# Optimization experiments

Hardware: AMD Instinct MI355X
Metric: run time of the kernel (lower is better)

The kernel has to match this reference:

```python
import jax, jax.numpy as jnp
import numpy as np

N, E = 50000, 800000          # nodes, edges
IN_CH, HID, HEADS = 256, 32, 4  # conv1: 256 -> 32x4; conv2: 128 -> 128 (1 head)
NEG_SLOPE = 0.2               # PyG GATConv default LeakyReLU slope


def setup_inputs() -> dict:
    key = jax.random.key(0)
    ks = jax.random.split(key, 9)
    H1 = HID * HEADS
    p = lambda k, shape, s: jax.random.normal(k, shape, jnp.float32) * s
    return {
        "x": jax.random.normal(ks[0], (N, IN_CH), jnp.float32),
        "src": jax.random.randint(ks[1], (E,), 0, N, dtype=jnp.int32),
        "dst": jax.random.randint(ks[2], (E,), 0, N, dtype=jnp.int32),
        "W1": p(ks[3], (IN_CH, H1), (2.0 / IN_CH) ** 0.5),
        "att_src1": p(ks[4], (HEADS, HID), 0.1),
        "att_dst1": p(ks[5], (HEADS, HID), 0.1),
        "b1": jnp.zeros((H1,), jnp.float32),
        "W2": p(ks[6], (H1, H1), (2.0 / H1) ** 0.5),
        "att_src2": p(ks[7], (1, H1), 0.1),
        "att_dst2": p(ks[8], (1, H1), 0.1),
        "b2": jnp.zeros((H1,), jnp.float32),
    }


def _gat_conv(x, src, dst, W, a_src, a_dst, b):
    """PyG-style GATConv: project, per-edge attention, segment softmax over dst, scatter-sum."""
    n = x.shape[0]
    H, C = a_src.shape
    xp = (x @ W).reshape(n, H, C)                      # [N,H,C]
    al_s = jnp.sum(xp * a_src, axis=-1)                # [N,H]
    al_d = jnp.sum(xp * a_dst, axis=-1)                # [N,H]
    e = jax.nn.leaky_relu(al_s[src] + al_d[dst], NEG_SLOPE)   # [E,H]
    m = jax.lax.stop_gradient(jax.ops.segment_max(e, dst, num_segments=n))
    ex = jnp.exp(e - m[dst])                           # stable segment softmax
    z = jax.ops.segment_sum(ex, dst, num_segments=n)
    alpha = ex / (z[dst] + 1e-16)                      # [E,H]
    out = jax.ops.segment_sum(xp[src] * alpha[..., None], dst, num_segments=n)
    return out.reshape(n, H * C) + b


def reference(x, src, dst, W1, att_src1, att_dst1, b1, W2, att_src2, att_dst2, b2):
    n = x.shape[0]
    loops = jnp.arange(n, dtype=src.dtype)             # add_self_loops=True (PyG default)
    s = jnp.concatenate([src, loops])
    d = jnp.concatenate([dst, loops])
    # eval mode: dropout is identity
    h = jax.nn.elu(_gat_conv(x, s, d, W1, att_src1, att_dst1, b1))
    return _gat_conv(h, s, d, W2, att_src2, att_dst2, b2)
```

## Files before the change

kernel.cpp:

```cpp
#include <hip/hip_runtime.h>

#define NN 50000
#define NE 800000
#define NEG 0.2f

constexpr int NB1 = (NN + 255) / 256;

__device__ __forceinline__ float lrelu(float x) { return x > 0.f ? x : NEG * x; }

__global__ void hist_k(const int* __restrict__ dst, int* __restrict__ deg) {
    int i = blockIdx.x * 256 + threadIdx.x;
    if (i < NE) atomicAdd(&deg[dst[i]], 1);
}

__global__ void scan1_k(const int* __restrict__ deg, int* __restrict__ roff,
                        int* __restrict__ bsum) {
    __shared__ int s[256];
    int t = threadIdx.x;
    int i = blockIdx.x * 256 + t;
    int v = (i < NN) ? deg[i] : 0;
    s[t] = v; __syncthreads();
    for (int off = 1; off < 256; off <<= 1) {
        int add = (t >= off) ? s[t - off] : 0;
        __syncthreads();
        s[t] += add;
        __syncthreads();
    }
    if (i < NN) roff[i] = s[t] - v;
    if (t == 255) bsum[blockIdx.x] = s[255];
}

__global__ void scan2_k(const int* __restrict__ bsum, int* __restrict__ boff,
                        int* __restrict__ roff) {
    __shared__ int s[256];
    int t = threadIdx.x;
    int v = (t < NB1) ? bsum[t] : 0;
    s[t] = v; __syncthreads();
    for (int off = 1; off < 256; off <<= 1) {
        int add = (t >= off) ? s[t - off] : 0;
        __syncthreads();
        s[t] += add;
        __syncthreads();
    }
    if (t < NB1) boff[t] = s[t] - v;
    if (t == 255) roff[NN] = s[255];
}

__global__ void scan3_k(int* __restrict__ roff, const int* __restrict__ boff,
                        int* __restrict__ cursor) {
    int i = blockIdx.x * 256 + threadIdx.x;
    if (i < NN) {
        int v = roff[i] + boff[blockIdx.x];
        roff[i] = v;
        cursor[i] = v;
    }
}

template <bool WITH_DST>
__global__ void fill_k(const int* __restrict__ src, const int* __restrict__ dst,
                       int* __restrict__ cursor, int* __restrict__ csr,
                       int* __restrict__ dstOf) {
    int i = blockIdx.x * 256 + threadIdx.x;
    if (i < NE) {
        int d = dst[i];
        int p = atomicAdd(&cursor[d], 1);
        csr[p] = src[i];
        if (WITH_DST) dstOf[p] = d;
    }
}

__global__ void wt1_k(const int* __restrict__ csr, const int* __restrict__ dstOf,
                      const float* __restrict__ als, const float* __restrict__ ald,
                      float* __restrict__ w) {
    int p = blockIdx.x * 256 + threadIdx.x;
    if (p >= NE) return;
    int s = csr[p], d = dstOf[p];
    float4 av = *reinterpret_cast<const float4*>(&als[s * 4]);
    float4 dv = *reinterpret_cast<const float4*>(&ald[d * 4]);
    float4 wv;
    wv.x = __expf(lrelu(av.x + dv.x));
    wv.y = __expf(lrelu(av.y + dv.y));
    wv.z = __expf(lrelu(av.z + dv.z));
    wv.w = __expf(lrelu(av.w + dv.w));
    *reinterpret_cast<float4*>(&w[(size_t)p * 4]) = wv;
}

__global__ void wt2_k(const int* __restrict__ csr, const int* __restrict__ dstOf,
                      const float* __restrict__ als, const float* __restrict__ ald,
                      float* __restrict__ w) {
    int p = blockIdx.x * 256 + threadIdx.x;
    if (p >= NE) return;
    w[p] = __expf(lrelu(als[csr[p]] + ald[dstOf[p]]));
}

template <int K, int HEADS>
__global__ __launch_bounds__(256) void gemm_k(const float* __restrict__ A,
                                              const float* __restrict__ W,
                                              const float* __restrict__ att_s,
                                              const float* __restrict__ att_d,
                                              float* __restrict__ O,
                                              float* __restrict__ als,
                                              float* __restrict__ ald, int M) {
    __shared__ float sAT[32][68];
    __shared__ float sB[32][128];
    int row0 = blockIdx.x * 64;
    int t = threadIdx.x;
    int rg = t >> 5;
    int cg = t & 31;
    float acc[8][4] = {};
    for (int k0 = 0; k0 < K; k0 += 32) {
        #pragma unroll
        for (int p = 0; p < 2; ++p) {
            int r = p * 32 + (t >> 3);
            int kk4 = (t & 7) * 4;
            int gr = row0 + r;
            float4 v = make_float4(0.f, 0.f, 0.f, 0.f);
            if (gr < M) v = *reinterpret_cast<const float4*>(&A[(size_t)gr * K + k0 + kk4]);
            sAT[kk4 + 0][r] = v.x;
            sAT[kk4 + 1][r] = v.y;
            sAT[kk4 + 2][r] = v.z;
            sAT[kk4 + 3][r] = v.w;
        }
        #pragma unroll
        for (int p = 0; p < 4; ++p) {
            int kr = p * 8 + (t >> 5);
            int c4 = (t & 31) * 4;
            *reinterpret_cast<float4*>(&sB[kr][c4]) =
                *reinterpret_cast<const float4*>(&W[(size_t)(k0 + kr) * 128 + c4]);
        }
        __syncthreads();
        #pragma unroll
        for (int kk = 0; kk < 32; ++kk) {
            float4 a0 = *reinterpret_cast<const float4*>(&sAT[kk][rg * 8]);
            float4 a1 = *reinterpret_cast<const float4*>(&sAT[kk][rg * 8 + 4]);
            float4 bv = *reinterpret_cast<const float4*>(&sB[kk][cg * 4]);
            float ar[8] = {a0.x, a0.y, a0.z, a0.w, a1.x, a1.y, a1.z, a1.w};
            #pragma unroll
            for (int r = 0; r < 8; ++r) {
                acc[r][0] += ar[r] * bv.x;
                acc[r][1] += ar[r] * bv.y;
                acc[r][2] += ar[r] * bv.z;
                acc[r][3] += ar[r] * bv.w;
            }
        }
        __syncthreads();
    }
    constexpr int GROUP = 32 / HEADS;
    float4 as4 = *reinterpret_cast<const float4*>(&att_s[cg * 4]);
    float4 ad4 = *reinterpret_cast<const float4*>(&att_d[cg * 4]);
    #pragma unroll
    for (int r = 0; r < 8; ++r) {
        int gr = row0 + rg * 8 + r;
        float4 o = make_float4(acc[r][0], acc[r][1], acc[r][2], acc[r][3]);
        float ps = o.x * as4.x + o.y * as4.y + o.z * as4.z + o.w * as4.w;
        float pd = o.x * ad4.x + o.y * ad4.y + o.z * ad4.z + o.w * ad4.w;
        #pragma unroll
        for (int m = 1; m < GROUP; m <<= 1) {
            ps += __shfl_xor(ps, m, 64);
            pd += __shfl_xor(pd, m, 64);
        }
        if (gr < M) {
            *reinterpret_cast<float4*>(&O[(size_t)gr * 128 + cg * 4]) = o;
            if ((cg & (GROUP - 1)) == 0) {
                int h = cg / GROUP;
                als[(size_t)gr * HEADS + h] = ps;
                ald[(size_t)gr * HEADS + h] = pd;
            }
        }
    }
}

template <int HEADS>
__global__ __launch_bounds__(256) void aggf_k(const int* __restrict__ roff,
                                              const int* __restrict__ csr,
                                              const float* __restrict__ w,
                                              const float* __restrict__ xp,
                                              const float* __restrict__ als,
                                              const float* __restrict__ ald,
                                              const float* __restrict__ b,
                                              float* __restrict__ outp, int doElu) {
    int node = (blockIdx.x * 256 + threadIdx.x) >> 6;
    int lane = threadIdx.x & 63;
    if (node >= NN) return;
    int hw = lane >> 5;
    int l  = lane & 31;
    int h  = (HEADS == 4) ? (l >> 3) : 0;
    int e0 = roff[node], e1 = roff[node + 1];

    float selfw;
    if (HEADS == 4) {
        float4 adv = *reinterpret_cast<const float4*>(&ald[node * 4]);
        float4 sv  = *reinterpret_cast<const float4*>(&als[node * 4]);
        float adh = (h == 0) ? adv.x : (h == 1) ? adv.y : (h == 2) ? adv.z : adv.w;
        float svh = (h == 0) ? sv.x  : (h == 1) ? sv.y  : (h == 2) ? sv.z  : sv.w;
        selfw = __expf(lrelu(svh + adh));
    } else {
        selfw = __expf(lrelu(als[node] + ald[node]));
    }

    float aA0 = 0.f, aA1 = 0.f, aA2 = 0.f, aA3 = 0.f, zA = 0.f;
    float aB0 = 0.f, aB1 = 0.f, aB2 = 0.f, aB3 = 0.f, zB = 0.f;
    if (hw == 0) {
        zA = selfw;
        float4 v = *reinterpret_cast<const float4*>(&xp[(size_t)node * 128 + 4 * l]);
        aA0 = selfw * v.x; aA1 = selfw * v.y; aA2 = selfw * v.z; aA3 = selfw * v.w;
    }
    for (int j = e0 + hw; j < e1; j += 8) {
        int i1 = j + 2, i2 = j + 4, i3 = j + 6;
        bool p1 = i1 < e1, p2 = i2 < e1, p3 = i3 < e1;
        int j1 = p1 ? i1 : j, j2 = p2 ? i2 : j, j3 = p3 ? i3 : j;
        int s0 = csr[j], s1 = csr[j1], s2 = csr[j2], s3 = csr[j3];
        float w0, w1v, w2v, w3v;
        if (HEADS == 4) {
            w0  = w[(size_t)j  * 4 + h];
            w1v = w[(size_t)j1 * 4 + h];
            w2v = w[(size_t)j2 * 4 + h];
            w3v = w[(size_t)j3 * 4 + h];
        } else {
            w0 = w[j]; w1v = w[j1]; w2v = w[j2]; w3v = w[j3];
        }
        w1v = p1 ? w1v : 0.f;
        w2v = p2 ? w2v : 0.f;
        w3v = p3 ? w3v : 0.f;
        float4 v0 = *reinterpret_cast<const float4*>(&xp[(size_t)s0 * 128 + 4 * l]);
        float4 v1 = *reinterpret_cast<const float4*>(&xp[(size_t)s1 * 128 + 4 * l]);
        float4 v2 = *reinterpret_cast<const float4*>(&xp[(size_t)s2 * 128 + 4 * l]);
        float4 v3 = *reinterpret_cast<const float4*>(&xp[(size_t)s3 * 128 + 4 * l]);
        zA += w0;  aA0 += w0 * v0.x;  aA1 += w0 * v0.y;  aA2 += w0 * v0.z;  aA3 += w0 * v0.w;
        zA += w1v; aA0 += w1v * v1.x; aA1 += w1v * v1.y; aA2 += w1v * v1.z; aA3 += w1v * v1.w;
        zB += w2v; aB0 += w2v * v2.x; aB1 += w2v * v2.y; aB2 += w2v * v2.z; aB3 += w2v * v2.w;
        zB += w3v; aB0 += w3v * v3.x; aB1 += w3v * v3.y; aB2 += w3v * v3.z; aB3 += w3v * v3.w;
    }
    float a0 = aA0 + aB0, a1 = aA1 + aB1, a2 = aA2 + aB2, a3 = aA3 + aB3, z = zA + zB;
    a0 += __shfl_xor(a0, 32, 64);
    a1 += __shfl_xor(a1, 32, 64);
    a2 += __shfl_xor(a2, 32, 64);
    a3 += __shfl_xor(a3, 32, 64);
    z  += __shfl_xor(z, 32, 64);
    if (hw == 0) {
        float inv = 1.f / (z + 1e-16f);
        float4 bb = *reinterpret_cast<const float4*>(&b[4 * l]);
        float o0 = a0 * inv + bb.x, o1 = a1 * inv + bb.y;
        float o2 = a2 * inv + bb.z, o3 = a3 * inv + bb.w;
        if (doElu) {
            o0 = o0 > 0.f ? o0 : expm1f(o0);
            o1 = o1 > 0.f ? o1 : expm1f(o1);
            o2 = o2 > 0.f ? o2 : expm1f(o2);
            o3 = o3 > 0.f ? o3 : expm1f(o3);
        }
        *reinterpret_cast<float4*>(&outp[(size_t)node * 128 + 4 * l]) =
            make_float4(o0, o1, o2, o3);
    }
}

__global__ __launch_bounds__(256) void agg1_k(const int* __restrict__ roff,
                                              const int* __restrict__ csr,
                                              const float* __restrict__ xp,
                                              const float* __restrict__ als,
                                              const float* __restrict__ ald,
                                              const float* __restrict__ b,
                                              float* __restrict__ hout) {
    int node = (blockIdx.x * 256 + threadIdx.x) >> 6;
    int lane = threadIdx.x & 63;
    if (node >= NN) return;
    int hw = lane >> 5;
    int l  = lane & 31;
    int h  = l >> 3;
    int e0 = roff[node], e1 = roff[node + 1];

    float4 adv = *reinterpret_cast<const float4*>(&ald[node * 4]);
    float4 sv  = *reinterpret_cast<const float4*>(&als[node * 4]);
    float adh = (h == 0) ? adv.x : (h == 1) ? adv.y : (h == 2) ? adv.z : adv.w;
    float svh = (h == 0) ? sv.x  : (h == 1) ? sv.y  : (h == 2) ? sv.z  : sv.w;

    float aA0 = 0.f, aA1 = 0.f, aA2 = 0.f, aA3 = 0.f, zA = 0.f;
    float aB0 = 0.f, aB1 = 0.f, aB2 = 0.f, aB3 = 0.f, zB = 0.f;
    if (hw == 0) {
        float ex = __expf(lrelu(svh + adh));
        zA = ex;
        float4 v = *reinterpret_cast<const float4*>(&xp[(size_t)node * 128 + 4 * l]);
        aA0 = ex * v.x; aA1 = ex * v.y; aA2 = ex * v.z; aA3 = ex * v.w;
    }
    for (int j = e0 + hw; j < e1; j += 4) {
        int sA = csr[j];
        int jB = j + 2;
        bool hasB = jB < e1;
        int sB = hasB ? csr[jB] : sA;
        float4 avA = *reinterpret_cast<const float4*>(&als[sA * 4]);
        float4 avB = *reinterpret_cast<const float4*>(&als[sB * 4]);
        float alA = (h == 0) ? avA.x : (h == 1) ? avA.y : (h == 2) ? avA.z : avA.w;
        float alB = (h == 0) ? avB.x : (h == 1) ? avB.y : (h == 2) ? avB.z : avB.w;
        float exA = __expf(lrelu(alA + adh));
        float exB = hasB ? __expf(lrelu(alB + adh)) : 0.f;
        float4 vA = *reinterpret_cast<const float4*>(&xp[(size_t)sA * 128 + 4 * l]);
        float4 vB = *reinterpret_cast<const float4*>(&xp[(size_t)sB * 128 + 4 * l]);
        zA += exA; aA0 += exA * vA.x; aA1 += exA * vA.y; aA2 += exA * vA.z; aA3 += exA * vA.w;
        zB += exB; aB0 += exB * vB.x; aB1 += exB * vB.y; aB2 += exB * vB.z; aB3 += exB * vB.w;
    }
    float a0 = aA0 + aB0, a1 = aA1 + aB1, a2 = aA2 + aB2, a3 = aA3 + aB3, z = zA + zB;
    a0 += __shfl_xor(a0, 32, 64);
    a1 += __shfl_xor(a1, 32, 64);
    a2 += __shfl_xor(a2, 32, 64);
    a3 += __shfl_xor(a3, 32, 64);
    z  += __shfl_xor(z, 32, 64);
    if (hw == 0) {
        float inv = 1.f / (z + 1e-16f);
        float4 bb = *reinterpret_cast<const float4*>(&b[4 * l]);
        float o0 = a0 * inv + bb.x, o1 = a1 * inv + bb.y;
        float o2 = a2 * inv + bb.z, o3 = a3 * inv + bb.w;
        o0 = o0 > 0.f ? o0 : expm1f(o0);
        o1 = o1 > 0.f ? o1 : expm1f(o1);
        o2 = o2 > 0.f ? o2 : expm1f(o2);
        o3 = o3 > 0.f ? o3 : expm1f(o3);
        *reinterpret_cast<float4*>(&hout[(size_t)node * 128 + 4 * l]) =
            make_float4(o0, o1, o2, o3);
    }
}

__global__ __launch_bounds__(256) void agg2_k(const int* __restrict__ roff,
                                              const int* __restrict__ csr,
                                              const float* __restrict__ xp,
                                              const float* __restrict__ als,
                                              const float* __restrict__ ald,
                                              const float* __restrict__ b,
                                              float* __restrict__ out) {
    int node = (blockIdx.x * 256 + threadIdx.x) >> 6;
    int lane = threadIdx.x & 63;
    if (node >= NN) return;
    int hw = lane >> 5;
    int l  = lane & 31;
    int e0 = roff[node], e1 = roff[node + 1];
    float ad = ald[node];
    float sl = als[node];

    float aA0 = 0.f, aA1 = 0.f, aA2 = 0.f, aA3 = 0.f, zA = 0.f;
    float aB0 = 0.f, aB1 = 0.f, aB2 = 0.f, aB3 = 0.f, zB = 0.f;
    if (hw == 0) {
        float ex = __expf(lrelu(sl + ad));
        zA = ex;
        float4 v = *reinterpret_cast<const float4*>(&xp[(size_t)node * 128 + 4 * l]);
        aA0 = ex * v.x; aA1 = ex * v.y; aA2 = ex * v.z; aA3 = ex * v.w;
    }
    for (int j = e0 + hw; j < e1; j += 4) {
        int sA = csr[j];
        int jB = j + 2;
        bool hasB = jB < e1;
        int sB = hasB ? csr[jB] : sA;
        float alA = als[sA];
        float alB = als[sB];
        float exA = __expf(lrelu(alA + ad));
        float exB = hasB ? __expf(lrelu(alB + ad)) : 0.f;
        float4 vA = *reinterpret_cast<const float4*>(&xp[(size_t)sA * 128 + 4 * l]);
        float4 vB = *reinterpret_cast<const float4*>(&xp[(size_t)sB * 128 + 4 * l]);
        zA += exA; aA0 += exA * vA.x; aA1 += exA * vA.y; aA2 += exA * vA.z; aA3 += exA * vA.w;
        zB += exB; aB0 += exB * vB.x; aB1 += exB * vB.y; aB2 += exB * vB.z; aB3 += exB * vB.w;
    }
    float a0 = aA0 + aB0, a1 = aA1 + aB1, a2 = aA2 + aB2, a3 = aA3 + aB3, z = zA + zB;
    a0 += __shfl_xor(a0, 32, 64);
    a1 += __shfl_xor(a1, 32, 64);
    a2 += __shfl_xor(a2, 32, 64);
    a3 += __shfl_xor(a3, 32, 64);
    z  += __shfl_xor(z, 32, 64);
    if (hw == 0) {
        float inv = 1.f / (z + 1e-16f);
        float4 bb = *reinterpret_cast<const float4*>(&b[4 * l]);
        *reinterpret_cast<float4*>(&out[(size_t)node * 128 + 4 * l]) =
            make_float4(a0 * inv + bb.x, a1 * inv + bb.y, a2 * inv + bb.z, a3 * inv + bb.w);
    }
}

extern "C" void kernel_launch(void* const* d_in, const int* in_sizes, int n_in,
                              void* d_out, int out_size, void* d_ws, size_t ws_size,
                              hipStream_t stream) {
    const float* x   = (const float*)d_in[0];
    const int*   src = (const int*)d_in[1];
    const int*   dst = (const int*)d_in[2];
    const float* W1  = (const float*)d_in[3];
    const float* as1 = (const float*)d_in[4];
    const float* ad1 = (const float*)d_in[5];
    const float* b1  = (const float*)d_in[6];
    const float* W2  = (const float*)d_in[7];
    const float* as2 = (const float*)d_in[8];
    const float* ad2 = (const float*)d_in[9];
    const float* b2  = (const float*)d_in[10];
    float* out = (float*)d_out;

    char* ws = (char*)d_ws;
    size_t off = 0;
    auto alloc = [&](size_t bytes) {
        size_t o = off;
        off = (off + bytes + 255) & ~(size_t)255;
        return o;
    };
    int*   roff   = (int*)(ws + alloc((NN + 1) * 4));
    int*   cursor = (int*)(ws + alloc(NN * 4));
    int*   deg    = (int*)(ws + alloc(NN * 4));
    int*   bsum   = (int*)(ws + alloc(256 * 4));
    int*   boff   = (int*)(ws + alloc(256 * 4));
    int*   csr    = (int*)(ws + alloc((size_t)NE * 4));
    float* xp1    = (float*)(ws + alloc((size_t)NN * 128 * 4));
    float* als1   = (float*)(ws + alloc((size_t)NN * 4 * 4));
    float* ald1   = (float*)(ws + alloc((size_t)NN * 4 * 4));
    float* hbuf   = (float*)(ws + alloc((size_t)NN * 128 * 4));
    int*   dstOf  = (int*)(ws + alloc((size_t)NE * 4));
    float* w1     = (float*)(ws + alloc((size_t)NE * 4 * 4));
    float* w2     = w1;
    bool fast = (off <= ws_size);

    float* xp2  = xp1;
    float* als2 = als1;
    float* ald2 = ald1;

    hipMemsetAsync(deg, 0, (size_t)NN * 4, stream);
    hist_k<<<(NE + 255) / 256, 256, 0, stream>>>(dst, deg);
    scan1_k<<<NB1, 256, 0, stream>>>(deg, roff, bsum);
    scan2_k<<<1, 256, 0, stream>>>(bsum, boff, roff);
    scan3_k<<<NB1, 256, 0, stream>>>(roff, boff, cursor);
    int eGrid = (NE + 255) / 256;
    if (fast) fill_k<true><<<eGrid, 256, 0, stream>>>(src, dst, cursor, csr, dstOf);
    else      fill_k<false><<<eGrid, 256, 0, stream>>>(src, dst, cursor, csr, dstOf);

    int aggGrid  = (NN + 3) / 4;
    int gemmGrid = (NN + 63) / 64;

    gemm_k<256, 4><<<gemmGrid, 256, 0, stream>>>(x, W1, as1, ad1, xp1, als1, ald1, NN);
    if (fast) {
        wt1_k<<<eGrid, 256, 0, stream>>>(csr, dstOf, als1, ald1, w1);
        aggf_k<4><<<aggGrid, 256, 0, stream>>>(roff, csr, w1, xp1, als1, ald1, b1, hbuf, 1);
    } else {
        agg1_k<<<aggGrid, 256, 0, stream>>>(roff, csr, xp1, als1, ald1, b1, hbuf);
    }

    gemm_k<128, 1><<<gemmGrid, 256, 0, stream>>>(hbuf, W2, as2, ad2, xp2, als2, ald2, NN);
    if (fast) {
        wt2_k<<<eGrid, 256, 0, stream>>>(csr, dstOf, als2, ald2, w2);
        aggf_k<1><<<aggGrid, 256, 0, stream>>>(roff, csr, w2, xp2, als2, ald2, b2, out, 0);
    } else {
        agg2_k<<<aggGrid, 256, 0, stream>>>(roff, csr, xp2, als2, ald2, b2, out);
    }
}
```

Baseline: 408.1 us.

## Replace FP32 projection GEMMs with split-bf16 MFMA GEMMs

Adds a kernel that pre-splits each weight matrix into high and low bf16 parts, transposed. The projection GEMMs then run on MFMA 16x16x32 bf16 instructions using three products (hi*hi, lo*hi, hi*lo), which recovers near-FP32 accuracy, and the attention dot-products are fused into the epilogue. The aim is to replace the scalar FP32 GEMM path with matrix-core throughput. In exchange it adds per-call bf16 splitting of the activations and weights, extra LDS traffic, and two small weight-split launches, with slightly lower precision than true FP32.

```diff
diff --git a/kernel.cpp b/kernel.cpp
--- a/kernel.cpp
+++ b/kernel.cpp
@@ -7,6 +7,14 @@
 constexpr int NB1 = (NN + 255) / 256;
 
 __device__ __forceinline__ float lrelu(float x) { return x > 0.f ? x : NEG * x; }
+
+typedef __attribute__((ext_vector_type(8))) short short8v;
+typedef __attribute__((ext_vector_type(4))) float f32x4;
+
+__device__ __forceinline__ ushort f2bf(float x) {
+    unsigned u = __float_as_uint(x);
+    return (ushort)((u + 0x7FFFu + ((u >> 16) & 1u)) >> 16);
+}
 
 __global__ void hist_k(const int* __restrict__ dst, int* __restrict__ deg) {
     int i = blockIdx.x * 256 + threadIdx.x;
@@ -67,6 +75,19 @@
         csr[p] = src[i];
         if (WITH_DST) dstOf[p] = d;
     }
+}
+
+__global__ void wsplit_k(const float* __restrict__ W, ushort* __restrict__ WTh,
+                         ushort* __restrict__ WTl, int K) {
+    int idx = blockIdx.x * 256 + threadIdx.x;
+    if (idx >= K * 128) return;
+    int c = idx / K;
+    int k = idx - c * K;
+    float v = W[(size_t)k * 128 + c];
+    ushort h = f2bf(v);
+    float hf = __uint_as_float(((unsigned)h) << 16);
+    WTh[idx] = h;
+    WTl[idx] = f2bf(v - hf);
 }
 
 __global__ void wt1_k(const int* __restrict__ csr, const int* __restrict__ dstOf,
@@ -91,6 +112,131 @@
     int p = blockIdx.x * 256 + threadIdx.x;
     if (p >= NE) return;
     w[p] = __expf(lrelu(als[csr[p]] + ald[dstOf[p]]));
+}
+
+template <int K, int HEADS>
+__global__ __launch_bounds__(256) void gemm_mfma_k(const float* __restrict__ A,
+                                                   const ushort* __restrict__ WTh,
+                                                   const ushort* __restrict__ WTl,
+                                                   const float* __restrict__ att_s,
+                                                   const float* __restrict__ att_d,
+                                                   float* __restrict__ O,
+                                                   float* __restrict__ als,
+                                                   float* __restrict__ ald, int M) {
+    __shared__ ushort sAh[64][40];
+    __shared__ ushort sAl[64][40];
+    __shared__ ushort sWh[128][40];
+    __shared__ ushort sWl[128][40];
+    int t = threadIdx.x;
+    int w = t >> 6;
+    int l = t & 63;
+    int r16 = l & 15, kg = l >> 4;
+    int row0 = blockIdx.x * 64;
+
+    f32x4 acc[8] = {};
+
+    for (int k0 = 0; k0 < K; k0 += 32) {
+        #pragma unroll
+        for (int p = 0; p < 2; ++p) {
+            int idx = p * 256 + t;
+            int r = idx >> 3, kk = (idx & 7) * 4;
+            int gr = row0 + r;
+            float4 v = make_float4(0.f, 0.f, 0.f, 0.f);
+            if (gr < M) v = *reinterpret_cast<const float4*>(&A[(size_t)gr * K + k0 + kk]);
+            ushort h0 = f2bf(v.x), h1 = f2bf(v.y), h2 = f2bf(v.z), h3 = f2bf(v.w);
+            short4 hv = make_short4((short)h0, (short)h1, (short)h2, (short)h3);
+            float f0 = __uint_as_float(((unsigned)h0) << 16);
+            float f1 = __uint_as_float(((unsigned)h1) << 16);
+            float f2 = __uint_as_float(((unsigned)h2) << 16);
+            float f3 = __uint_as_float(((unsigned)h3) << 16);
+            short4 lv = make_short4((short)f2bf(v.x - f0), (short)f2bf(v.y - f1),
+                                    (short)f2bf(v.z - f2), (short)f2bf(v.w - f3));
+            *reinterpret_cast<short4*>(&sAh[r][kk]) = hv;
+            *reinterpret_cast<short4*>(&sAl[r][kk]) = lv;
+        }
+        {
+            int c = t & 127, kh = (t >> 7) * 16;
+            const int4* gh = reinterpret_cast<const int4*>(&WTh[(size_t)c * K + k0 + kh]);
+            const int4* gl = reinterpret_cast<const int4*>(&WTl[(size_t)c * K + k0 + kh]);
+            int4 a0 = gh[0], a1 = gh[1];
+            int4 b0 = gl[0], b1 = gl[1];
+            *reinterpret_cast<int4*>(&sWh[c][kh])     = a0;
+            *reinterpret_cast<int4*>(&sWh[c][kh + 8]) = a1;
+            *reinterpret_cast<int4*>(&sWl[c][kh])     = b0;
+            *reinterpret_cast<int4*>(&sWl[c][kh + 8]) = b1;
+        }
+        __syncthreads();
+        short8v ah = *reinterpret_cast<const short8v*>(&sAh[w * 16 + r16][kg * 8]);
+        short8v al_ = *reinterpret_cast<const short8v*>(&sAl[w * 16 + r16][kg * 8]);
+        #pragma unroll
+        for (int ct = 0; ct < 8; ++ct) {
+            short8v bh = *reinterpret_cast<const short8v*>(&sWh[ct * 16 + r16][kg * 8]);
+            short8v bl = *reinterpret_cast<const short8v*>(&sWl[ct * 16 + r16][kg * 8]);
+            acc[ct] = __builtin_amdgcn_mfma_f32_16x16x32_bf16(ah,  bh, acc[ct], 0, 0, 0);
+            acc[ct] = __builtin_amdgcn_mfma_f32_16x16x32_bf16(al_, bh, acc[ct], 0, 0, 0);
+            acc[ct] = __builtin_amdgcn_mfma_f32_16x16x32_bf16(ah,  bl, acc[ct], 0, 0, 0);
+        }
+        __syncthreads();
+    }
+
+    float asv[8], adv[8];
+    #pragma unroll
+    for (int ct = 0; ct < 8; ++ct) {
+        asv[ct] = att_s[ct * 16 + r16];
+        adv[ct] = att_d[ct * 16 + r16];
+    }
+    #pragma unroll
+    for (int i = 0; i < 4; ++i) {
+        int gr = row0 + w * 16 + kg * 4 + i;
+        if (HEADS == 4) {
+            float p0 = 0.f, p1 = 0.f, p2 = 0.f, p3 = 0.f;
+            float q0 = 0.f, q1 = 0.f, q2 = 0.f, q3 = 0.f;
+            #pragma unroll
+            for (int ct = 0; ct < 8; ++ct) {
+                float a = acc[ct][i];
+                if (ct < 2)      { p0 += a * asv[ct]; q0 += a * adv[ct]; }
+                else if (ct < 4) { p1 += a * asv[ct]; q1 += a * adv[ct]; }
+                else if (ct < 6) { p2 += a * asv[ct]; q2 += a * adv[ct]; }
+                else             { p3 += a * asv[ct]; q3 += a * adv[ct]; }
+            }
+            #pragma unroll
+            for (int m = 1; m < 16; m <<= 1) {
+                p0 += __shfl_xor(p0, m, 64); p1 += __shfl_xor(p1, m, 64);
+                p2 += __shfl_xor(p2, m, 64); p3 += __shfl_xor(p3, m, 64);
+                q0 += __shfl_xor(q0, m, 64); q1 += __shfl_xor(q1, m, 64);
+                q2 += __shfl_xor(q2, m, 64); q3 += __shfl_xor(q3, m, 64);
+            }
+            if (gr < M) {
+                #pragma unroll
+                for (int ct = 0; ct < 8; ++ct)
+                    O[(size_t)gr * 128 + ct * 16 + r16] = acc[ct][i];
+                if (r16 == 0) {
+                    als[(size_t)gr * 4 + 0] = p0; als[(size_t)gr * 4 + 1] = p1;
+                    als[(size_t)gr * 4 + 2] = p2; als[(size_t)gr * 4 + 3] = p3;
+                    ald[(size_t)gr * 4 + 0] = q0; ald[(size_t)gr * 4 + 1] = q1;
+                    ald[(size_t)gr * 4 + 2] = q2; ald[(size_t)gr * 4 + 3] = q3;
+                }
+            }
+        } else {
+            float p = 0.f, q = 0.f;
+            #pragma unroll
+            for (int ct = 0; ct < 8; ++ct) {
+                float a = acc[ct][i];
+                p += a * asv[ct]; q += a * adv[ct];
+            }
+            #pragma unroll
+            for (int m = 1; m < 16; m <<= 1) {
+                p += __shfl_xor(p, m, 64);
+                q += __shfl_xor(q, m, 64);
+            }
+            if (gr < M) {
+                #pragma unroll
+                for (int ct = 0; ct < 8; ++ct)
+                    O[(size_t)gr * 128 + ct * 16 + r16] = acc[ct][i];
+                if (r16 == 0) { als[gr] = p; ald[gr] = q; }
+            }
+        }
+    }
 }
 
 template <int K, int HEADS>
@@ -267,12 +413,10 @@
     int l  = lane & 31;
     int h  = l >> 3;
     int e0 = roff[node], e1 = roff[node + 1];
-
     float4 adv = *reinterpret_cast<const float4*>(&ald[node * 4]);
     float4 sv  = *reinterpret_cast<const float4*>(&als[node * 4]);
     float adh = (h == 0) ? adv.x : (h == 1) ? adv.y : (h == 2) ? adv.z : adv.w;
     float svh = (h == 0) ? sv.x  : (h == 1) ? sv.y  : (h == 2) ? sv.z  : sv.w;
-
     float aA0 = 0.f, aA1 = 0.f, aA2 = 0.f, aA3 = 0.f, zA = 0.f;
     float aB0 = 0.f, aB1 = 0.f, aB2 = 0.f, aB3 = 0.f, zB = 0.f;
     if (hw == 0) {
@@ -332,7 +476,6 @@
     int e0 = roff[node], e1 = roff[node + 1];
     float ad = ald[node];
     float sl = als[node];
-
     float aA0 = 0.f, aA1 = 0.f, aA2 = 0.f, aA3 = 0.f, zA = 0.f;
     float aB0 = 0.f, aB1 = 0.f, aB2 = 0.f, aB3 = 0.f, zB = 0.f;
     if (hw == 0) {
@@ -402,9 +545,13 @@
     float* als1   = (float*)(ws + alloc((size_t)NN * 4 * 4));
     float* ald1   = (float*)(ws + alloc((size_t)NN * 4 * 4));
     float* hbuf   = (float*)(ws + alloc((size_t)NN * 128 * 4));
-    int*   dstOf  = (int*)(ws + alloc((size_t)NE * 4));
-    float* w1     = (float*)(ws + alloc((size_t)NE * 4 * 4));
-    float* w2     = w1;
+    int*    dstOf = (int*)(ws + alloc((size_t)NE * 4));
+    float*  w1    = (float*)(ws + alloc((size_t)NE * 4 * 4));
+    ushort* wt1h  = (ushort*)(ws + alloc((size_t)128 * 256 * 2));
+    ushort* wt1l  = (ushort*)(ws + alloc((size_t)128 * 256 * 2));
+    ushort* wt2h  = (ushort*)(ws + alloc((size_t)128 * 128 * 2));
+    ushort* wt2l  = (ushort*)(ws + alloc((size_t)128 * 128 * 2));
+    float* w2 = w1;
     bool fast = (off <= ws_size);
 
     float* xp2  = xp1;
@@ -423,19 +570,21 @@
     int aggGrid  = (NN + 3) / 4;
     int gemmGrid = (NN + 63) / 64;
 
-    gemm_k<256, 4><<<gemmGrid, 256, 0, stream>>>(x, W1, as1, ad1, xp1, als1, ald1, NN);
     if (fast) {
+        wsplit_k<<<(256 * 128 + 255) / 256, 256, 0, stream>>>(W1, wt1h, wt1l, 256);
+        wsplit_k<<<(128 * 128 + 255) / 256, 256, 0, stream>>>(W2, wt2h, wt2l, 128);
+        gemm_mfma_k<256, 4><<<gemmGrid, 256, 0, stream>>>(x, wt1h, wt1l, as1, ad1,
+                                                          xp1, als1, ald1, NN);
         wt1_k<<<eGrid, 256, 0, stream>>>(csr, dstOf, als1, ald1, w1);
         aggf_k<4><<<aggGrid, 256, 0, stream>>>(roff, csr, w1, xp1, als1, ald1, b1, hbuf, 1);
-    } else {
-        agg1_k<<<aggGrid, 256, 0, stream>>>(roff, csr, xp1, als1, ald1, b1, hbuf);
-    }
-
-    gemm_k<128, 1><<<gemmGrid, 256, 0, stream>>>(hbuf, W2, as2, ad2, xp2, als2, ald2, NN);
-    if (fast) {
+        gemm_mfma_k<128, 1><<<gemmGrid, 256, 0, stream>>>(hbuf, wt2h, wt2l, as2, ad2,
+                                                          xp2, als2, ald2, NN);
         wt2_k<<<eGrid, 256, 0, stream>>>(csr, dstOf, als2, ald2, w2);
         aggf_k<1><<<aggGrid, 256, 0, stream>>>(roff, csr, w2, xp2, als2, ald2, b2, out, 0);
     } else {
+        gemm_k<256, 4><<<gemmGrid, 256, 0, stream>>>(x, W1, as1, ad1, xp1, als1, ald1, NN);
+        agg1_k<<<aggGrid, 256, 0, stream>>>(roff, csr, xp1, als1, ald1, b1, hbuf);
+        gemm_k<128, 1><<<gemmGrid, 256, 0, stream>>>(hbuf, W2, as2, ad2, xp2, als2, ald2, NN);
         agg2_k<<<aggGrid, 256, 0, stream>>>(roff, csr, xp2, als2, ald2, b2, out);
     }
 }
```

New measurement: 378.3 us. 7.3% less time.
